# Kernel optimization log

Measured on AMD Instinct MI355X. Metric: run time of the kernel, lower is better.

The kernel has to match this reference:

```python
import jax, jax.numpy as jnp
import numpy as np

B, N, H, OUT, L = 32, 4096, 256, 256, 4
EPS = 1e-5


def _build_edge_index(num_nodes):
    grid = int(np.sqrt(num_nodes)) + 1
    edges = []
    for i in range(num_nodes):
        col = i % grid
        if col < grid - 1 and i + 1 < num_nodes:
            edges.append([i, i + 1]); edges.append([i + 1, i])
        if i + grid < num_nodes:
            edges.append([i, i + grid]); edges.append([i + grid, i])
    return np.asarray(edges, dtype=np.int64).T  # [2, E]


def setup_inputs() -> dict:
    key = jax.random.key(0)
    ks = jax.random.split(key, 12)
    s = 0.02
    x = (jax.random.uniform(ks[0], (B, N)) < 0.1).astype(jnp.float32)  # syndrome bits
    edge_index = jnp.asarray(_build_edge_index(N))
    return {
        "x": x,
        "edge_index": edge_index,
        "proj_w": jax.random.normal(ks[1], (1, H)) * s,
        "proj_b": jnp.zeros((H,)),
        "conv_w": jax.random.normal(ks[2], (L, H, H)) * s,
        "conv_b": jnp.zeros((L, H)),
        "ln_g": jnp.ones((L, H)),
        "ln_b": jnp.zeros((L, H)),
        "h1_w": jax.random.normal(ks[3], (H, H)) * s,
        "h1_b": jnp.zeros((H,)),
        "h2_w": jax.random.normal(ks[4], (H, OUT)) * s,
        "h2_b": jnp.zeros((OUT,)),
    }


def reference(x, edge_index, proj_w, proj_b, conv_w, conv_b, ln_g, ln_b,
              h1_w, h1_b, h2_w, h2_b):
    batch, n = x.shape
    total = batch * n
    # batched edge index: replicate per sample with node offsets
    offsets = (jnp.arange(batch, dtype=edge_index.dtype) * n)
    ei = (edge_index[:, None, :] + offsets[None, :, None]).reshape(2, -1)
    src, dst = ei[0], ei[1]

    h = x.reshape(total, 1) @ proj_w + proj_b  # [total, H]

    # GCN symmetric norm with self-loops (degree = in-degree + 1)
    deg = jnp.zeros((total,), h.dtype).at[dst].add(1.0) + 1.0
    dinv_sqrt = jax.lax.rsqrt(deg)
    enorm = (dinv_sqrt[src] * dinv_sqrt[dst])[:, None]  # [E, 1]
    self_norm = (1.0 / deg)[:, None]                    # [total, 1]

    for l in range(L):
        t = h @ conv_w[l]                                   # transform
        agg = jnp.zeros_like(t).at[dst].add(enorm * t[src])  # scatter-add
        t = agg + self_norm * t + conv_b[l]
        mu = t.mean(-1, keepdims=True)
        var = ((t - mu) ** 2).mean(-1, keepdims=True)
        t = (t - mu) * jax.lax.rsqrt(var + EPS) * ln_g[l] + ln_b[l]
        h = jax.nn.relu(t)

    pooled = h.reshape(batch, n, -1).mean(axis=1)  # global_mean_pool (equal-size graphs)
    return jax.nn.relu(pooled @ h1_w + h1_b) @ h2_w + h2_b
```

## Files before the change

### kernel.cpp

```cpp
#include <hip/hip_runtime.h>
#include <cstdint>
#include <cstddef>

#define TOTAL (32*4096)
#define H 256
#define NLAYER 4

typedef _Float16 f16x8 __attribute__((ext_vector_type(8)));
typedef _Float16 f16x4 __attribute__((ext_vector_type(4)));
typedef float floatx4 __attribute__((ext_vector_type(4)));

__device__ __forceinline__ float dinv_of(int n) {
  int col = n % 65;
  int deg = 1;
  deg += (n >= 1 && col != 0) ? 1 : 0;
  deg += (col != 64 && n <= 4094) ? 1 : 0;
  deg += (n >= 65) ? 1 : 0;
  deg += (n <= 4030) ? 1 : 0;
  return rsqrtf((float)deg);
}

__device__ __forceinline__ void loadf8(const float* p, float* v) {
  float4 a = *reinterpret_cast<const float4*>(p);
  float4 b = *reinterpret_cast<const float4*>(p + 4);
  v[0] = a.x; v[1] = a.y; v[2] = a.z; v[3] = a.w;
  v[4] = b.x; v[5] = b.y; v[6] = b.z; v[7] = b.w;
}

__global__ void k_transpose(const float* __restrict__ src,
                            unsigned short* __restrict__ wt,
                            float* __restrict__ pooled) {
  int idx = blockIdx.x * 256 + threadIdx.x;
  if (blockIdx.x < 32) pooled[idx] = 0.0f;
  int n = idx & 255;
  int k = (idx >> 8) & 255;
  int l = idx >> 16;
  int wgrp = n >> 6, cc = n & 3, ll = (n >> 2) & 15;
  int ngrp = wgrp * 4 + cc;
  int c = k >> 5, lq = (k >> 3) & 3, j = k & 7;
  _Float16 hv = (_Float16)src[idx];
  union { _Float16 h; unsigned short u; } pk; pk.h = hv;
  wt[(size_t)l * 65536 + (ngrp * 8 + c) * 512 + (lq * 16 + ll) * 8 + j] = pk.u;
}

template <int AGG, int POOL, int GPROJ>
__global__ __launch_bounds__(512, 4)
void k_gemm_ln(const _Float16* __restrict__ Hin,
               const float* __restrict__ x,
               const float* __restrict__ pw,
               const float* __restrict__ pb,
               const _Float16* __restrict__ Bf,
               const float* __restrict__ cb,
               const float* __restrict__ lg,
               const float* __restrict__ lb,
               _Float16* __restrict__ Hout,
               float* __restrict__ pooled) {
  __shared__ alignas(16) unsigned char smem_u[128 * 130 * 4];
  _Float16* As = reinterpret_cast<_Float16*>(smem_u);
  float*    p2 = reinterpret_cast<float*>(smem_u);
  __shared__ float red2[4][128][2];
  __shared__ float musr[128][4];
  const int t = threadIdx.x;
  const int w = t >> 6, lane = t & 63;
  const int lq = lane >> 4, ll = lane & 15;
  const int wm = w & 1;
  const int wcg = w >> 1;
  const int tile = (blockIdx.x & 7) * (gridDim.x >> 3) + (blockIdx.x >> 3);
  const int m0 = tile * 128;
  const int ar = t >> 2;
  const int aq = t & 3;

  {
    const int gi = m0 + ar;
    const int nd = gi & 4095;
    const int col = nd % 65;
    const float di = dinv_of(nd);
    const int key = (ar & 7) << 3;
    if (GPROJ) {
      const int base = gi - nd;
      float sx = di * x[gi];
      float sc = di;
      if (nd >= 1 && col != 0)     { float dj = dinv_of(nd - 1);  sx += dj * x[base + nd - 1];  sc += dj; }
      if (col != 64 && nd <= 4094) { float dj = dinv_of(nd + 1);  sx += dj * x[base + nd + 1];  sc += dj; }
      if (nd >= 65)                { float dj = dinv_of(nd - 65); sx += dj * x[base + nd - 65]; sc += dj; }
      if (nd <= 4030)              { float dj = dinv_of(nd + 65); sx += dj * x[base + nd + 65]; sc += dj; }
      sx *= di; sc *= di;
#pragma unroll
      for (int q = 0; q < 8; q++) {
        const int k0 = q * 32 + aq * 8;
        float wv[8], bv[8];
        loadf8(pw + k0, wv);
        loadf8(pb + k0, bv);
        f16x8 oh;
#pragma unroll
        for (int j = 0; j < 8; j++) oh[j] = (_Float16)(sx * wv[j] + sc * bv[j]);
        *reinterpret_cast<f16x8*>(&As[ar * 256 + (((q * 4 + aq) * 8) ^ key)]) = oh;
      }
    } else {
      const _Float16 dih = (_Float16)di;
      _Float16 m1 = (_Float16)0.f, m2 = (_Float16)0.f, m3 = (_Float16)0.f, m4 = (_Float16)0.f;
      const _Float16* r0p = Hin + (size_t)gi * 256 + aq * 8;
      const _Float16* r1p = r0p;
      const _Float16* r2p = r0p;
      const _Float16* r3p = r0p;
      const _Float16* r4p = r0p;
      if (nd >= 1 && col != 0)     { r1p = r0p - 256;      m1 = (_Float16)1.f; }
      if (col != 64 && nd <= 4094) { r2p = r0p + 256;      m2 = (_Float16)1.f; }
      if (nd >= 65)                { r3p = r0p - 65 * 256; m3 = (_Float16)1.f; }
      if (nd <= 4030)              { r4p = r0p + 65 * 256; m4 = (_Float16)1.f; }
#pragma unroll
      for (int q = 0; q < 8; q++) {
        const int k0 = q * 32;
        f16x8 a0 = *reinterpret_cast<const f16x8*>(r0p + k0);
        f16x8 a1 = *reinterpret_cast<const f16x8*>(r1p + k0);
        f16x8 a2 = *reinterpret_cast<const f16x8*>(r2p + k0);
        f16x8 a3 = *reinterpret_cast<const f16x8*>(r3p + k0);
        f16x8 a4 = *reinterpret_cast<const f16x8*>(r4p + k0);
        f16x8 o = (a0 + a1 * m1 + a2 * m2 + a3 * m3 + a4 * m4) * dih;
        *reinterpret_cast<f16x8*>(&As[ar * 256 + (((q * 4 + aq) * 8) ^ key)]) = o;
      }
    }
  }
  __syncthreads();

  floatx4 acc[4][4] = {};
  const _Float16* bbase = Bf + (size_t)(wcg * 4) * 8 * 512 + lane * 8;
  const int rkey = (ll & 7) << 3;
  const int rowbase = wm * 64;

#pragma unroll
  for (int c = 0; c < 8; c++) {
    f16x8 bfr[4], af[4];
#pragma unroll
    for (int cc = 0; cc < 4; cc++)
      bfr[cc] = *reinterpret_cast<const f16x8*>(bbase + (cc * 8 + c) * 512);
#pragma unroll
    for (int r = 0; r < 4; r++)
      af[r] = *reinterpret_cast<const f16x8*>(
          &As[(rowbase + r * 16 + ll) * 256 + (((c * 4 + lq) << 3) ^ rkey)]);
#pragma unroll
    for (int r = 0; r < 4; r++)
#pragma unroll
      for (int cc = 0; cc < 4; cc++)
        acc[r][cc] = __builtin_amdgcn_mfma_f32_16x16x32_f16(af[r], bfr[cc], acc[r][cc], 0, 0, 0);
  }

  const int colbase = wcg * 64 + (ll << 2);
  const float4 cb4 = *reinterpret_cast<const float4*>(cb + colbase);
  const float4 lg4 = *reinterpret_cast<const float4*>(lg + colbase);
  const float4 lb4 = *reinterpret_cast<const float4*>(lb + colbase);
  const float cbv[4]  = {cb4.x, cb4.y, cb4.z, cb4.w};
  const float gamv[4] = {lg4.x, lg4.y, lg4.z, lg4.w};
  const float betv[4] = {lb4.x, lb4.y, lb4.z, lb4.w};

  __syncthreads();
  {
    const int slice2 = (wcg * 16 + ll) * 2;
#pragma unroll
    for (int r = 0; r < 4; r++) {
#pragma unroll
      for (int reg = 0; reg < 4; reg++) {
        float sv = 0.f, sq = 0.f;
#pragma unroll
        for (int c = 0; c < 4; c++) {
          float v = acc[r][c][reg] + cbv[c];
          sv += v; sq += v * v;
        }
        const int row = rowbase + r * 16 + lq * 4 + reg;
        *reinterpret_cast<float2*>(&p2[row * 130 + slice2]) = make_float2(sv, sq);
      }
    }
  }
  __syncthreads();
  {
    const int row = t & 127, tq = t >> 7;
    float s = 0.f, q = 0.f;
#pragma unroll
    for (int i = 0; i < 16; i++) {
      float2 pq = *reinterpret_cast<const float2*>(&p2[row * 130 + (tq * 16 + i) * 2]);
      s += pq.x; q += pq.y;
    }
    red2[tq][row][0] = s;
    red2[tq][row][1] = q;
  }
  __syncthreads();
  if (t < 128) {
    float s = red2[0][t][0] + red2[1][t][0] + red2[2][t][0] + red2[3][t][0];
    float q = red2[0][t][1] + red2[1][t][1] + red2[2][t][1] + red2[3][t][1];
    float mu = s * (1.0f / 256.0f);
    float var = fmaxf(q * (1.0f / 256.0f) - mu * mu, 0.0f);
    musr[t][0] = mu;
    musr[t][1] = rsqrtf(var + 1e-5f);
    musr[t][2] = dinv_of((m0 + t) & 4095);
  }
  __syncthreads();

  if (POOL == 0) {
#pragma unroll
    for (int r = 0; r < 4; r++) {
#pragma unroll
      for (int reg = 0; reg < 4; reg++) {
        int row = rowbase + r * 16 + lq * 4 + reg;
        float mu = musr[row][0], rsg = musr[row][1], dr = musr[row][2];
        f16x4 st;
#pragma unroll
        for (int c = 0; c < 4; c++) {
          float v = (acc[r][c][reg] + cbv[c] - mu) * rsg * gamv[c] + betv[c];
          st[c] = (_Float16)(fmaxf(v, 0.0f) * dr);
        }
        *reinterpret_cast<f16x4*>(&Hout[(size_t)(m0 + row) * 256 + colbase]) = st;
      }
    }
  } else {
    float csum[4] = {0.f, 0.f, 0.f, 0.f};
#pragma unroll
    for (int r = 0; r < 4; r++) {
#pragma unroll
      for (int reg = 0; reg < 4; reg++) {
        int row = rowbase + r * 16 + lq * 4 + reg;
        float mu = musr[row][0], rsg = musr[row][1];
#pragma unroll
        for (int c = 0; c < 4; c++) {
          float hv = (acc[r][c][reg] + cbv[c] - mu) * rsg * gamv[c] + betv[c];
          csum[c] += fmaxf(hv, 0.0f);
        }
      }
    }
#pragma unroll
    for (int c = 0; c < 4; c++) {
      csum[c] += __shfl_xor(csum[c], 16, 64);
      csum[c] += __shfl_xor(csum[c], 32, 64);
    }
    if (lq == 0) {
      int b = m0 >> 12;
#pragma unroll
      for (int c = 0; c < 4; c++)
        atomicAdd(&pooled[b * 256 + colbase + c], csum[c] * (1.0f / 4096.0f));
    }
  }
}

__global__ void k_head(const float* __restrict__ pooled,
                       const float* __restrict__ w1,
                       const float* __restrict__ b1,
                       const float* __restrict__ w2,
                       const float* __restrict__ b2,
                       float* __restrict__ out) {
  const int b = blockIdx.x;
  const int t = threadIdx.x;
  __shared__ float row[256];
  __shared__ float y1[256];
  row[t] = pooled[b * 256 + t];
  __syncthreads();
  float s = b1[t];
#pragma unroll 8
  for (int k = 0; k < 256; k++) s += row[k] * w1[k * 256 + t];
  y1[t] = fmaxf(s, 0.0f);
  __syncthreads();
  float s2 = b2[t];
#pragma unroll 8
  for (int k = 0; k < 256; k++) s2 += y1[k] * w2[k * 256 + t];
  out[b * 256 + t] = s2;
}

extern "C" void kernel_launch(void* const* d_in, const int* in_sizes, int n_in,
                              void* d_out, int out_size, void* d_ws, size_t ws_size,
                              hipStream_t stream) {
  (void)in_sizes; (void)n_in; (void)out_size; (void)ws_size;
  const float* x      = (const float*)d_in[0];
  const float* proj_w = (const float*)d_in[2];
  const float* proj_b = (const float*)d_in[3];
  const float* conv_w = (const float*)d_in[4];
  const float* conv_b = (const float*)d_in[5];
  const float* ln_g   = (const float*)d_in[6];
  const float* ln_b   = (const float*)d_in[7];
  const float* h1_w   = (const float*)d_in[8];
  const float* h1_b   = (const float*)d_in[9];
  const float* h2_w   = (const float*)d_in[10];
  const float* h2_b   = (const float*)d_in[11];

  char* ws = (char*)d_ws;
  const size_t act_bytes = (size_t)TOTAL * H * 2;
  _Float16* ha     = (_Float16*)ws;
  _Float16* hb     = (_Float16*)(ws + act_bytes);
  unsigned short* wt_u = (unsigned short*)(ws + 2 * act_bytes);
  _Float16* wt     = (_Float16*)wt_u;
  float*    pooled = (float*)(ws + 2 * act_bytes + (size_t)NLAYER * H * H * 2);

  k_transpose<<<NLAYER * H * H / 256, 256, 0, stream>>>(conv_w, wt_u, pooled);

  const int GB = TOTAL / 128;
  k_gemm_ln<0, 0, 1><<<GB, 512, 0, stream>>>(nullptr, x, proj_w, proj_b,
      wt + 0 * (size_t)H * H, conv_b + 0 * H, ln_g + 0 * H, ln_b + 0 * H, hb, nullptr);
  k_gemm_ln<1, 0, 0><<<GB, 512, 0, stream>>>(hb, nullptr, nullptr, nullptr,
      wt + 1 * (size_t)H * H, conv_b + 1 * H, ln_g + 1 * H, ln_b + 1 * H, ha, nullptr);
  k_gemm_ln<1, 0, 0><<<GB, 512, 0, stream>>>(ha, nullptr, nullptr, nullptr,
      wt + 2 * (size_t)H * H, conv_b + 2 * H, ln_g + 2 * H, ln_b + 2 * H, hb, nullptr);
  k_gemm_ln<1, 1, 0><<<GB, 512, 0, stream>>>(hb, nullptr, nullptr, nullptr,
      wt + 3 * (size_t)H * H, conv_b + 3 * H, ln_g + 3 * H, ln_b + 3 * H, nullptr, pooled);

  k_head<<<32, 256, 0, stream>>>(pooled, h1_w, h1_b, h2_w, h2_b, (float*)d_out);
}
```

Baseline: 267.9 us.

## Fuse all layers into one persistent kernel with atomic grid barriers

Replaces the six separate launches (weight transpose, four GEMM+LayerNorm layers, head MLP) with a single persistent kernel of 512 blocks. Each block handles two row tiles per layer, and an atomic-counter grid barrier separates the phases. The aim is to remove kernel launch gaps and per-launch tail effects. In exchange it depends on all 512 blocks being co-resident to avoid deadlock, adds spin-wait barrier cost, and runs the head on only 32 blocks while the rest sit idle.

```diff
diff --git a/kernel.cpp b/kernel.cpp
--- a/kernel.cpp
+++ b/kernel.cpp
@@ -5,6 +5,7 @@
 #define TOTAL (32*4096)
 #define H 256
 #define NLAYER 4
+#define NB 512
 
 typedef _Float16 f16x8 __attribute__((ext_vector_type(8)));
 typedef _Float16 f16x4 __attribute__((ext_vector_type(4)));
@@ -27,240 +28,269 @@
   v[4] = b.x; v[5] = b.y; v[6] = b.z; v[7] = b.w;
 }
 
-__global__ void k_transpose(const float* __restrict__ src,
-                            unsigned short* __restrict__ wt,
-                            float* __restrict__ pooled) {
-  int idx = blockIdx.x * 256 + threadIdx.x;
-  if (blockIdx.x < 32) pooled[idx] = 0.0f;
-  int n = idx & 255;
-  int k = (idx >> 8) & 255;
-  int l = idx >> 16;
-  int wgrp = n >> 6, cc = n & 3, ll = (n >> 2) & 15;
-  int ngrp = wgrp * 4 + cc;
-  int c = k >> 5, lq = (k >> 3) & 3, j = k & 7;
-  _Float16 hv = (_Float16)src[idx];
-  union { _Float16 h; unsigned short u; } pk; pk.h = hv;
-  wt[(size_t)l * 65536 + (ngrp * 8 + c) * 512 + (lq * 16 + ll) * 8 + j] = pk.u;
-}
-
-template <int AGG, int POOL, int GPROJ>
+__device__ __forceinline__ void gridbar(unsigned* bar, unsigned target) {
+  __syncthreads();
+  if (threadIdx.x == 0) {
+    __threadfence();
+    __hip_atomic_fetch_add(bar, 1u, __ATOMIC_ACQ_REL, __HIP_MEMORY_SCOPE_AGENT);
+    while (__hip_atomic_load(bar, __ATOMIC_ACQUIRE, __HIP_MEMORY_SCOPE_AGENT) < target)
+      __builtin_amdgcn_s_sleep(2);
+    __threadfence();
+  }
+  __syncthreads();
+}
+
 __global__ __launch_bounds__(512, 4)
-void k_gemm_ln(const _Float16* __restrict__ Hin,
-               const float* __restrict__ x,
-               const float* __restrict__ pw,
-               const float* __restrict__ pb,
-               const _Float16* __restrict__ Bf,
-               const float* __restrict__ cb,
-               const float* __restrict__ lg,
-               const float* __restrict__ lb,
-               _Float16* __restrict__ Hout,
-               float* __restrict__ pooled) {
+void k_all(const float* __restrict__ x,
+           const float* __restrict__ proj_w, const float* __restrict__ proj_b,
+           const float* __restrict__ conv_w, const float* __restrict__ conv_b,
+           const float* __restrict__ ln_g, const float* __restrict__ ln_b,
+           const float* __restrict__ h1_w, const float* __restrict__ h1_b,
+           const float* __restrict__ h2_w, const float* __restrict__ h2_b,
+           float* out,
+           _Float16* ha, _Float16* hb,
+           unsigned short* wt_u, float* pooled,
+           unsigned* bar) {
   __shared__ alignas(16) unsigned char smem_u[128 * 130 * 4];
   _Float16* As = reinterpret_cast<_Float16*>(smem_u);
   float*    p2 = reinterpret_cast<float*>(smem_u);
   __shared__ float red2[4][128][2];
   __shared__ float musr[128][4];
+
   const int t = threadIdx.x;
+  const int bid = blockIdx.x;
   const int w = t >> 6, lane = t & 63;
   const int lq = lane >> 4, ll = lane & 15;
   const int wm = w & 1;
   const int wcg = w >> 1;
-  const int tile = (blockIdx.x & 7) * (gridDim.x >> 3) + (blockIdx.x >> 3);
-  const int m0 = tile * 128;
   const int ar = t >> 2;
   const int aq = t & 3;
+  const int rowbase = wm * 64;
+  const int rkey = (ll & 7) << 3;
+  const int colbase = wcg * 64 + (ll << 2);
 
   {
-    const int gi = m0 + ar;
-    const int nd = gi & 4095;
-    const int col = nd % 65;
-    const float di = dinv_of(nd);
-    const int key = (ar & 7) << 3;
-    if (GPROJ) {
-      const int base = gi - nd;
-      float sx = di * x[gi];
-      float sc = di;
-      if (nd >= 1 && col != 0)     { float dj = dinv_of(nd - 1);  sx += dj * x[base + nd - 1];  sc += dj; }
-      if (col != 64 && nd <= 4094) { float dj = dinv_of(nd + 1);  sx += dj * x[base + nd + 1];  sc += dj; }
-      if (nd >= 65)                { float dj = dinv_of(nd - 65); sx += dj * x[base + nd - 65]; sc += dj; }
-      if (nd <= 4030)              { float dj = dinv_of(nd + 65); sx += dj * x[base + nd + 65]; sc += dj; }
-      sx *= di; sc *= di;
-#pragma unroll
-      for (int q = 0; q < 8; q++) {
-        const int k0 = q * 32 + aq * 8;
-        float wv[8], bv[8];
-        loadf8(pw + k0, wv);
-        loadf8(pb + k0, bv);
-        f16x8 oh;
-#pragma unroll
-        for (int j = 0; j < 8; j++) oh[j] = (_Float16)(sx * wv[j] + sc * bv[j]);
-        *reinterpret_cast<f16x8*>(&As[ar * 256 + (((q * 4 + aq) * 8) ^ key)]) = oh;
-      }
-    } else {
-      const _Float16 dih = (_Float16)di;
-      _Float16 m1 = (_Float16)0.f, m2 = (_Float16)0.f, m3 = (_Float16)0.f, m4 = (_Float16)0.f;
-      const _Float16* r0p = Hin + (size_t)gi * 256 + aq * 8;
-      const _Float16* r1p = r0p;
-      const _Float16* r2p = r0p;
-      const _Float16* r3p = r0p;
-      const _Float16* r4p = r0p;
-      if (nd >= 1 && col != 0)     { r1p = r0p - 256;      m1 = (_Float16)1.f; }
-      if (col != 64 && nd <= 4094) { r2p = r0p + 256;      m2 = (_Float16)1.f; }
-      if (nd >= 65)                { r3p = r0p - 65 * 256; m3 = (_Float16)1.f; }
-      if (nd <= 4030)              { r4p = r0p + 65 * 256; m4 = (_Float16)1.f; }
-#pragma unroll
-      for (int q = 0; q < 8; q++) {
-        const int k0 = q * 32;
-        f16x8 a0 = *reinterpret_cast<const f16x8*>(r0p + k0);
-        f16x8 a1 = *reinterpret_cast<const f16x8*>(r1p + k0);
-        f16x8 a2 = *reinterpret_cast<const f16x8*>(r2p + k0);
-        f16x8 a3 = *reinterpret_cast<const f16x8*>(r3p + k0);
-        f16x8 a4 = *reinterpret_cast<const f16x8*>(r4p + k0);
-        f16x8 o = (a0 + a1 * m1 + a2 * m2 + a3 * m3 + a4 * m4) * dih;
-        *reinterpret_cast<f16x8*>(&As[ar * 256 + (((q * 4 + aq) * 8) ^ key)]) = o;
-      }
+    int idx = bid * 512 + t;
+    if (idx < 32 * 256) pooled[idx] = 0.0f;
+    int n = idx & 255;
+    int k = (idx >> 8) & 255;
+    int l = idx >> 16;
+    int wgrp = n >> 6, cc = n & 3, lll = (n >> 2) & 15;
+    int ngrp = wgrp * 4 + cc;
+    int c = k >> 5, lqq = (k >> 3) & 3, j = k & 7;
+    _Float16 hv = (_Float16)conv_w[idx];
+    union { _Float16 h; unsigned short u; } pk; pk.h = hv;
+    wt_u[(size_t)l * 65536 + (ngrp * 8 + c) * 512 + (lqq * 16 + lll) * 8 + j] = pk.u;
+  }
+  unsigned phase = 1;
+  gridbar(bar, phase * NB);
+
+  const _Float16* wt = reinterpret_cast<const _Float16*>(wt_u);
+
+  for (int l = 0; l < NLAYER; l++) {
+    const _Float16* Bf = wt + (size_t)l * 65536;
+    const float* cbp = conv_b + (l << 8);
+    const float* lgp = ln_g + (l << 8);
+    const float* lbp = ln_b + (l << 8);
+    const int gproj = (l == 0);
+    const int pool  = (l == 3);
+    const _Float16* Hin = (l == 1 || l == 3) ? hb : ha;
+    _Float16* Hout      = (l == 0 || l == 2) ? hb : ha;
+    const _Float16* bbase = Bf + (size_t)(wcg * 4) * 8 * 512 + lane * 8;
+
+    for (int rep = 0; rep < 2; rep++) {
+      const int v = bid + (rep << 9);
+      const int tile = (v & 7) * 128 + (v >> 3);
+      const int m0 = tile * 128;
+
+      {
+        const int gi = m0 + ar;
+        const int nd = gi & 4095;
+        const int colg = nd % 65;
+        const float di = dinv_of(nd);
+        const int key = (ar & 7) << 3;
+        if (gproj) {
+          const int base = gi - nd;
+          float sx = di * x[gi];
+          float sc = di;
+          if (nd >= 1 && colg != 0)     { float dj = dinv_of(nd - 1);  sx += dj * x[base + nd - 1];  sc += dj; }
+          if (colg != 64 && nd <= 4094) { float dj = dinv_of(nd + 1);  sx += dj * x[base + nd + 1];  sc += dj; }
+          if (nd >= 65)                 { float dj = dinv_of(nd - 65); sx += dj * x[base + nd - 65]; sc += dj; }
+          if (nd <= 4030)               { float dj = dinv_of(nd + 65); sx += dj * x[base + nd + 65]; sc += dj; }
+          sx *= di; sc *= di;
+#pragma unroll
+          for (int q = 0; q < 8; q++) {
+            const int k0 = q * 32 + aq * 8;
+            float wv[8], bv[8];
+            loadf8(proj_w + k0, wv);
+            loadf8(proj_b + k0, bv);
+            f16x8 oh;
+#pragma unroll
+            for (int j = 0; j < 8; j++) oh[j] = (_Float16)(sx * wv[j] + sc * bv[j]);
+            *reinterpret_cast<f16x8*>(&As[ar * 256 + (((q * 4 + aq) * 8) ^ key)]) = oh;
+          }
+        } else {
+          const _Float16 dih = (_Float16)di;
+          _Float16 m1 = (_Float16)0.f, m2 = (_Float16)0.f, m3 = (_Float16)0.f, m4 = (_Float16)0.f;
+          const _Float16* r0p = Hin + (size_t)gi * 256 + aq * 8;
+          const _Float16* r1p = r0p;
+          const _Float16* r2p = r0p;
+          const _Float16* r3p = r0p;
+          const _Float16* r4p = r0p;
+          if (nd >= 1 && colg != 0)     { r1p = r0p - 256;      m1 = (_Float16)1.f; }
+          if (colg != 64 && nd <= 4094) { r2p = r0p + 256;      m2 = (_Float16)1.f; }
+          if (nd >= 65)                 { r3p = r0p - 65 * 256; m3 = (_Float16)1.f; }
+          if (nd <= 4030)               { r4p = r0p + 65 * 256; m4 = (_Float16)1.f; }
+#pragma unroll
+          for (int q = 0; q < 8; q++) {
+            const int k0 = q * 32;
+            f16x8 a0 = *reinterpret_cast<const f16x8*>(r0p + k0);
+            f16x8 a1 = *reinterpret_cast<const f16x8*>(r1p + k0);
+            f16x8 a2 = *reinterpret_cast<const f16x8*>(r2p + k0);
+            f16x8 a3 = *reinterpret_cast<const f16x8*>(r3p + k0);
+            f16x8 a4 = *reinterpret_cast<const f16x8*>(r4p + k0);
+            f16x8 o = (a0 + a1 * m1 + a2 * m2 + a3 * m3 + a4 * m4) * dih;
+            *reinterpret_cast<f16x8*>(&As[ar * 256 + (((q * 4 + aq) * 8) ^ key)]) = o;
+          }
+        }
+      }
+      __syncthreads();
+
+      floatx4 acc[4][4] = {};
+#pragma unroll
+      for (int c = 0; c < 8; c++) {
+        f16x8 bfr[4], af[4];
+#pragma unroll
+        for (int cc = 0; cc < 4; cc++)
+          bfr[cc] = *reinterpret_cast<const f16x8*>(bbase + (cc * 8 + c) * 512);
+#pragma unroll
+        for (int r = 0; r < 4; r++)
+          af[r] = *reinterpret_cast<const f16x8*>(
+              &As[(rowbase + r * 16 + ll) * 256 + (((c * 4 + lq) << 3) ^ rkey)]);
+#pragma unroll
+        for (int r = 0; r < 4; r++)
+#pragma unroll
+          for (int cc = 0; cc < 4; cc++)
+            acc[r][cc] = __builtin_amdgcn_mfma_f32_16x16x32_f16(af[r], bfr[cc], acc[r][cc], 0, 0, 0);
+      }
+
+      const float4 cb4 = *reinterpret_cast<const float4*>(cbp + colbase);
+      const float4 lg4 = *reinterpret_cast<const float4*>(lgp + colbase);
+      const float4 lb4 = *reinterpret_cast<const float4*>(lbp + colbase);
+      const float cbv[4]  = {cb4.x, cb4.y, cb4.z, cb4.w};
+      const float gamv[4] = {lg4.x, lg4.y, lg4.z, lg4.w};
+      const float betv[4] = {lb4.x, lb4.y, lb4.z, lb4.w};
+
+      __syncthreads();
+      {
+        const int slice2 = (wcg * 16 + ll) * 2;
+#pragma unroll
+        for (int r = 0; r < 4; r++) {
+#pragma unroll
+          for (int reg = 0; reg < 4; reg++) {
+            float sv = 0.f, sq = 0.f;
+#pragma unroll
+            for (int c = 0; c < 4; c++) {
+              float vv = acc[r][c][reg] + cbv[c];
+              sv += vv; sq += vv * vv;
+            }
+            const int row = rowbase + r * 16 + lq * 4 + reg;
+            *reinterpret_cast<float2*>(&p2[row * 130 + slice2]) = make_float2(sv, sq);
+          }
+        }
+      }
+      __syncthreads();
+      {
+        const int row = t & 127, tq = t >> 7;
+        float s = 0.f, q = 0.f;
+#pragma unroll
+        for (int i = 0; i < 16; i++) {
+          float2 pq = *reinterpret_cast<const float2*>(&p2[row * 130 + (tq * 16 + i) * 2]);
+          s += pq.x; q += pq.y;
+        }
+        red2[tq][row][0] = s;
+        red2[tq][row][1] = q;
+      }
+      __syncthreads();
+      if (t < 128) {
+        float s = red2[0][t][0] + red2[1][t][0] + red2[2][t][0] + red2[3][t][0];
+        float q = red2[0][t][1] + red2[1][t][1] + red2[2][t][1] + red2[3][t][1];
+        float mu = s * (1.0f / 256.0f);
+        float var = fmaxf(q * (1.0f / 256.0f) - mu * mu, 0.0f);
+        musr[t][0] = mu;
+        musr[t][1] = rsqrtf(var + 1e-5f);
+        musr[t][2] = dinv_of((m0 + t) & 4095);
+      }
+      __syncthreads();
+
+      if (!pool) {
+#pragma unroll
+        for (int r = 0; r < 4; r++) {
+#pragma unroll
+          for (int reg = 0; reg < 4; reg++) {
+            int row = rowbase + r * 16 + lq * 4 + reg;
+            float mu = musr[row][0], rsg = musr[row][1], dr = musr[row][2];
+            f16x4 st;
+#pragma unroll
+            for (int c = 0; c < 4; c++) {
+              float vv = (acc[r][c][reg] + cbv[c] - mu) * rsg * gamv[c] + betv[c];
+              st[c] = (_Float16)(fmaxf(vv, 0.0f) * dr);
+            }
+            *reinterpret_cast<f16x4*>(&Hout[(size_t)(m0 + row) * 256 + colbase]) = st;
+          }
+        }
+      } else {
+        float csum[4] = {0.f, 0.f, 0.f, 0.f};
+#pragma unroll
+        for (int r = 0; r < 4; r++) {
+#pragma unroll
+          for (int reg = 0; reg < 4; reg++) {
+            int row = rowbase + r * 16 + lq * 4 + reg;
+            float mu = musr[row][0], rsg = musr[row][1];
+#pragma unroll
+            for (int c = 0; c < 4; c++) {
+              float hv = (acc[r][c][reg] + cbv[c] - mu) * rsg * gamv[c] + betv[c];
+              csum[c] += fmaxf(hv, 0.0f);
+            }
+          }
+        }
+#pragma unroll
+        for (int c = 0; c < 4; c++) {
+          csum[c] += __shfl_xor(csum[c], 16, 64);
+          csum[c] += __shfl_xor(csum[c], 32, 64);
+        }
+        if (lq == 0) {
+          int b = m0 >> 12;
+#pragma unroll
+          for (int c = 0; c < 4; c++)
+            atomicAdd(&pooled[b * 256 + colbase + c], csum[c] * (1.0f / 4096.0f));
+        }
+      }
+      __syncthreads();
+    }
+    phase++;
+    gridbar(bar, phase * NB);
+  }
+
+  if (bid < 32) {
+    float* rowv = p2;
+    float* y1v  = p2 + 256;
+    if (t < 256) rowv[t] = pooled[bid * 256 + t];
+    __syncthreads();
+    if (t < 256) {
+      float s = h1_b[t];
+#pragma unroll 8
+      for (int k = 0; k < 256; k++) s += rowv[k] * h1_w[k * 256 + t];
+      y1v[t] = fmaxf(s, 0.0f);
+    }
+    __syncthreads();
+    if (t < 256) {
+      float s2 = h2_b[t];
+#pragma unroll 8
+      for (int k = 0; k < 256; k++) s2 += y1v[k] * h2_w[k * 256 + t];
+      out[bid * 256 + t] = s2;
     }
   }
-  __syncthreads();
-
-  floatx4 acc[4][4] = {};
-  const _Float16* bbase = Bf + (size_t)(wcg * 4) * 8 * 512 + lane * 8;
-  const int rkey = (ll & 7) << 3;
-  const int rowbase = wm * 64;
-
-#pragma unroll
-  for (int c = 0; c < 8; c++) {
-    f16x8 bfr[4], af[4];
-#pragma unroll
-    for (int cc = 0; cc < 4; cc++)
-      bfr[cc] = *reinterpret_cast<const f16x8*>(bbase + (cc * 8 + c) * 512);
-#pragma unroll
-    for (int r = 0; r < 4; r++)
-      af[r] = *reinterpret_cast<const f16x8*>(
-          &As[(rowbase + r * 16 + ll) * 256 + (((c * 4 + lq) << 3) ^ rkey)]);
-#pragma unroll
-    for (int r = 0; r < 4; r++)
-#pragma unroll
-      for (int cc = 0; cc < 4; cc++)
-        acc[r][cc] = __builtin_amdgcn_mfma_f32_16x16x32_f16(af[r], bfr[cc], acc[r][cc], 0, 0, 0);
-  }
-
-  const int colbase = wcg * 64 + (ll << 2);
-  const float4 cb4 = *reinterpret_cast<const float4*>(cb + colbase);
-  const float4 lg4 = *reinterpret_cast<const float4*>(lg + colbase);
-  const float4 lb4 = *reinterpret_cast<const float4*>(lb + colbase);
-  const float cbv[4]  = {cb4.x, cb4.y, cb4.z, cb4.w};
-  const float gamv[4] = {lg4.x, lg4.y, lg4.z, lg4.w};
-  const float betv[4] = {lb4.x, lb4.y, lb4.z, lb4.w};
-
-  __syncthreads();
-  {
-    const int slice2 = (wcg * 16 + ll) * 2;
-#pragma unroll
-    for (int r = 0; r < 4; r++) {
-#pragma unroll
-      for (int reg = 0; reg < 4; reg++) {
-        float sv = 0.f, sq = 0.f;
-#pragma unroll
-        for (int c = 0; c < 4; c++) {
-          float v = acc[r][c][reg] + cbv[c];
-          sv += v; sq += v * v;
-        }
-        const int row = rowbase + r * 16 + lq * 4 + reg;
-        *reinterpret_cast<float2*>(&p2[row * 130 + slice2]) = make_float2(sv, sq);
-      }
-    }
-  }
-  __syncthreads();
-  {
-    const int row = t & 127, tq = t >> 7;
-    float s = 0.f, q = 0.f;
-#pragma unroll
-    for (int i = 0; i < 16; i++) {
-      float2 pq = *reinterpret_cast<const float2*>(&p2[row * 130 + (tq * 16 + i) * 2]);
-      s += pq.x; q += pq.y;
-    }
-    red2[tq][row][0] = s;
-    red2[tq][row][1] = q;
-  }
-  __syncthreads();
-  if (t < 128) {
-    float s = red2[0][t][0] + red2[1][t][0] + red2[2][t][0] + red2[3][t][0];
-    float q = red2[0][t][1] + red2[1][t][1] + red2[2][t][1] + red2[3][t][1];
-    float mu = s * (1.0f / 256.0f);
-    float var = fmaxf(q * (1.0f / 256.0f) - mu * mu, 0.0f);
-    musr[t][0] = mu;
-    musr[t][1] = rsqrtf(var + 1e-5f);
-    musr[t][2] = dinv_of((m0 + t) & 4095);
-  }
-  __syncthreads();
-
-  if (POOL == 0) {
-#pragma unroll
-    for (int r = 0; r < 4; r++) {
-#pragma unroll
-      for (int reg = 0; reg < 4; reg++) {
-        int row = rowbase + r * 16 + lq * 4 + reg;
-        float mu = musr[row][0], rsg = musr[row][1], dr = musr[row][2];
-        f16x4 st;
-#pragma unroll
-        for (int c = 0; c < 4; c++) {
-          float v = (acc[r][c][reg] + cbv[c] - mu) * rsg * gamv[c] + betv[c];
-          st[c] = (_Float16)(fmaxf(v, 0.0f) * dr);
-        }
-        *reinterpret_cast<f16x4*>(&Hout[(size_t)(m0 + row) * 256 + colbase]) = st;
-      }
-    }
-  } else {
-    float csum[4] = {0.f, 0.f, 0.f, 0.f};
-#pragma unroll
-    for (int r = 0; r < 4; r++) {
-#pragma unroll
-      for (int reg = 0; reg < 4; reg++) {
-        int row = rowbase + r * 16 + lq * 4 + reg;
-        float mu = musr[row][0], rsg = musr[row][1];
-#pragma unroll
-        for (int c = 0; c < 4; c++) {
-          float hv = (acc[r][c][reg] + cbv[c] - mu) * rsg * gamv[c] + betv[c];
-          csum[c] += fmaxf(hv, 0.0f);
-        }
-      }
-    }
-#pragma unroll
-    for (int c = 0; c < 4; c++) {
-      csum[c] += __shfl_xor(csum[c], 16, 64);
-      csum[c] += __shfl_xor(csum[c], 32, 64);
-    }
-    if (lq == 0) {
-      int b = m0 >> 12;
-#pragma unroll
-      for (int c = 0; c < 4; c++)
-        atomicAdd(&pooled[b * 256 + colbase + c], csum[c] * (1.0f / 4096.0f));
-    }
-  }
-}
-
-__global__ void k_head(const float* __restrict__ pooled,
-                       const float* __restrict__ w1,
-                       const float* __restrict__ b1,
-                       const float* __restrict__ w2,
-                       const float* __restrict__ b2,
-                       float* __restrict__ out) {
-  const int b = blockIdx.x;
-  const int t = threadIdx.x;
-  __shared__ float row[256];
-  __shared__ float y1[256];
-  row[t] = pooled[b * 256 + t];
-  __syncthreads();
-  float s = b1[t];
-#pragma unroll 8
-  for (int k = 0; k < 256; k++) s += row[k] * w1[k * 256 + t];
-  y1[t] = fmaxf(s, 0.0f);
-  __syncthreads();
-  float s2 = b2[t];
-#pragma unroll 8
-  for (int k = 0; k < 256; k++) s2 += y1[k] * w2[k * 256 + t];
-  out[b * 256 + t] = s2;
 }
 
 extern "C" void kernel_launch(void* const* d_in, const int* in_sizes, int n_in,
@@ -278,26 +308,20 @@
   const float* h1_b   = (const float*)d_in[9];
   const float* h2_w   = (const float*)d_in[10];
   const float* h2_b   = (const float*)d_in[11];
+  float* outp = (float*)d_out;
 
   char* ws = (char*)d_ws;
   const size_t act_bytes = (size_t)TOTAL * H * 2;
-  _Float16* ha     = (_Float16*)ws;
-  _Float16* hb     = (_Float16*)(ws + act_bytes);
+  _Float16* ha = (_Float16*)ws;
+  _Float16* hb = (_Float16*)(ws + act_bytes);
   unsigned short* wt_u = (unsigned short*)(ws + 2 * act_bytes);
-  _Float16* wt     = (_Float16*)wt_u;
-  float*    pooled = (float*)(ws + 2 * act_bytes + (size_t)NLAYER * H * H * 2);
-
-  k_transpose<<<NLAYER * H * H / 256, 256, 0, stream>>>(conv_w, wt_u, pooled);
-
-  const int GB = TOTAL / 128;
-  k_gemm_ln<0, 0, 1><<<GB, 512, 0, stream>>>(nullptr, x, proj_w, proj_b,
-      wt + 0 * (size_t)H * H, conv_b + 0 * H, ln_g + 0 * H, ln_b + 0 * H, hb, nullptr);
-  k_gemm_ln<1, 0, 0><<<GB, 512, 0, stream>>>(hb, nullptr, nullptr, nullptr,
-      wt + 1 * (size_t)H * H, conv_b + 1 * H, ln_g + 1 * H, ln_b + 1 * H, ha, nullptr);
-  k_gemm_ln<1, 0, 0><<<GB, 512, 0, stream>>>(ha, nullptr, nullptr, nullptr,
-      wt + 2 * (size_t)H * H, conv_b + 2 * H, ln_g + 2 * H, ln_b + 2 * H, hb, nullptr);
-  k_gemm_ln<1, 1, 0><<<GB, 512, 0, stream>>>(hb, nullptr, nullptr, nullptr,
-      wt + 3 * (size_t)H * H, conv_b + 3 * H, ln_g + 3 * H, ln_b + 3 * H, nullptr, pooled);
-
-  k_head<<<32, 256, 0, stream>>>(pooled, h1_w, h1_b, h2_w, h2_b, (float*)d_out);
-}
+  float* pooled = (float*)(ws + 2 * act_bytes + (size_t)NLAYER * H * H * 2);
+  unsigned* bar = (unsigned*)(ws + 2 * act_bytes + (size_t)NLAYER * H * H * 2
+                              + (size_t)32 * 256 * 4);
+
+  hipMemsetAsync(bar, 0, 64, stream);
+
+  k_all<<<NB, 512, 0, stream>>>(x, proj_w, proj_b, conv_w, conv_b,
+                                ln_g, ln_b, h1_w, h1_b, h2_w, h2_b,
+                                outp, ha, hb, wt_u, pooled, bar);
+}
```

Measured after the change: 880.3 us. 3.29x slower.
